# Optimization experiments

Measured on AMD Instinct MI355X. Metric: run time of the kernel, lower is better.

The kernel has to match this reference:

```python
import jax, jax.numpy as jnp
import numpy as np

B, T, D, HS = 4, 2048, 1024, 64

def setup_inputs() -> dict:
    key = jax.random.key(0)
    kx, kk, kq, kv = jax.random.split(key, 4)
    scale = 1.0 / np.sqrt(D)
    return {
        "x": jax.random.normal(kx, (B, T, D), dtype=jnp.float32),
        "Wk": jax.random.normal(kk, (D, HS), dtype=jnp.float32) * scale,
        "Wq": jax.random.normal(kq, (D, HS), dtype=jnp.float32) * scale,
        "Wv": jax.random.normal(kv, (D, HS), dtype=jnp.float32) * scale,
    }

def reference(x, Wk, Wq, Wv):
    # x: [B, T, D]; projections to [B, T, HS]
    k = jnp.einsum("btd,dh->bth", x, Wk)
    q = jnp.einsum("btd,dh->bth", x, Wq)
    v = jnp.einsum("btd,dh->bth", x, Wv)
    # scores [B, T, T]; NOTE: original multiplies by sqrt(head_size) (faithful)
    att = jnp.einsum("bth,bsh->bts", q, k) * jnp.sqrt(jnp.float32(k.shape[-1]))
    Tq = x.shape[1]
    causal = jnp.tril(jnp.ones((Tq, Tq), dtype=bool))
    att = jnp.where(causal[None, :, :], att, -jnp.inf)
    p = jax.nn.softmax(att, axis=-1)
    # dropout = identity (eval mode)
    return jnp.einsum("bts,bsh->bth", p, v)
```

## Files before the change

kernel.cpp:

```cpp
#include <hip/hip_runtime.h>

#define Bn 4
#define Tn 2048
#define Dn 1024
#define HSn 64

typedef __attribute__((ext_vector_type(8))) short bf16x8;
typedef __attribute__((ext_vector_type(4))) float f32x4;
typedef __attribute__((ext_vector_type(4))) short s16x4;
typedef unsigned short u16;
typedef unsigned int u32;

__device__ __forceinline__ u16 f2bf_rne(float x) {
    u32 u = __float_as_uint(x);
    return (u16)((u + 0x7FFFu + ((u >> 16) & 1u)) >> 16);
}
__device__ __forceinline__ u16 f2bf_trunc(float x) {
    return (u16)(__float_as_uint(x) >> 16);
}
__device__ __forceinline__ float bf2f(u16 h) {
    return __uint_as_float(((u32)h) << 16);
}

#define GLL16(g, l)                                                        \
    __builtin_amdgcn_global_load_lds(                                      \
        (const __attribute__((address_space(1))) void*)(g),                \
        (__attribute__((address_space(3))) void*)(l), 16, 0, 0)

__global__ __launch_bounds__(256) void wprep_kernel(
    const float* __restrict__ Wk, const float* __restrict__ Wq,
    const float* __restrict__ Wv, u16* __restrict__ wtp)
{
    __shared__ float ws_[64][65];
    const int kb = blockIdx.x;
    const int w  = blockIdx.y;
    const float* __restrict__ W = (w == 0) ? Wk : (w == 1) ? Wq : Wv;
    const float scale = (w == 1) ? 8.0f : 1.0f;
    const int t = threadIdx.x;

    {
        const int kl = t >> 2, hq = t & 3;
        #pragma unroll
        for (int i = 0; i < 4; ++i) {
            float4 f = *(const float4*)(W + (size_t)(kb * 64 + kl) * 64 + hq * 16 + i * 4);
            ws_[kl][hq * 16 + i * 4 + 0] = f.x; ws_[kl][hq * 16 + i * 4 + 1] = f.y;
            ws_[kl][hq * 16 + i * 4 + 2] = f.z; ws_[kl][hq * 16 + i * 4 + 3] = f.w;
        }
    }
    __syncthreads();

    const int h = t & 63, quarter = t >> 6;
    const int n = w * 64 + h;
    const int ks = kb * 2 + (quarter >> 1);
    const int k_in0 = (quarter & 1) * 16;
    u16 hib[16], lob[16];
    #pragma unroll
    for (int j = 0; j < 16; ++j) {
        float v = ws_[quarter * 16 + j][h] * scale;
        u16 hi = f2bf_trunc(v);
        hib[j] = hi;
        lob[j] = f2bf_trunc(v - bf2f(hi));
    }
    u16* dst = wtp + (size_t)n * 2048 + ks * 64;
    *(uint4*)(dst + k_in0)          = *(const uint4*)&hib[0];
    *(uint4*)(dst + k_in0 + 8)      = *(const uint4*)&hib[8];
    *(uint4*)(dst + 32 + k_in0)     = *(const uint4*)&lob[0];
    *(uint4*)(dst + 32 + k_in0 + 8) = *(const uint4*)&lob[8];
}

#define NKS 32
#define XB(P) (smem + (P) * 4096)
#define BB(P) (smem + 16384 + (P) * 12288)

__global__ __launch_bounds__(256) void proj_gemm(
    const float* __restrict__ x, const u16* __restrict__ wtp,
    u16* __restrict__ qh8, u16* __restrict__ ql8,
    u16* __restrict__ kth, u16* __restrict__ ktl,
    u16* __restrict__ vtt)
{
    __shared__ __align__(16) unsigned char smem[65536];

    const int tid  = threadIdx.x;
    const int wave = tid >> 6, lane = tid & 63;
    const int lo4  = lane & 15, g = lane >> 4;
    const int ch   = blockIdx.x >> 8;
    const int row0 = (blockIdx.x & 255) * 32;
    const int rt   = wave >> 1;
    const int cbase = (wave & 1) * 3;
    const int rl = rt * 16 + lo4;
    const int wcol0 = ch * 96;

    f32x4 acc[3];
    #pragma unroll
    for (int c = 0; c < 3; ++c) acc[c] = (f32x4){0.f, 0.f, 0.f, 0.f};

    const int xr = tid >> 3, xc = tid & 7;
    const int xsw = (xc ^ (xr & 7)) << 2;
    const float* xsrc0 = x + (size_t)(row0 + xr) * Dn + xsw;

    #define STAGE(P, KS)                                                     \
        {                                                                    \
            GLL16(xsrc0 + (KS) * 32, XB(P) + tid * 16);                      \
            _Pragma("unroll")                                                \
            for (int i = 0; i < 3; ++i) {                                    \
                const int c = i * 256 + tid;                                 \
                const int n_ = c >> 3, p_ = c & 7;                           \
                const int l_ = p_ ^ (n_ & 7);                                \
                const u16* src = wtp + (size_t)(wcol0 + n_) * 2048 + (KS) * 64 \
                                 + ((l_ & 3) << 3) + ((l_ >> 2) << 5);       \
                GLL16(src, BB(P) + c * 16);                                  \
            }                                                                \
        }

    #define COMPUTE(P, KS)                                                   \
        {                                                                    \
            bf16x8 ah, al;                                                   \
            {                                                                \
                const unsigned char* xb = XB(P) + rl * 128;                  \
                f32x4 f0 = *(const f32x4*)(xb + (((2 * g + 0) ^ (rl & 7)) << 4)); \
                f32x4 f1 = *(const f32x4*)(xb + (((2 * g + 1) ^ (rl & 7)) << 4)); \
                _Pragma("unroll")                                            \
                for (int jj = 0; jj < 4; ++jj) {                             \
                    u16 h0 = f2bf_trunc(f0[jj]);                             \
                    ah[jj] = (short)h0;                                      \
                    al[jj] = (short)f2bf_trunc(f0[jj] - bf2f(h0));           \
                    u16 h1 = f2bf_trunc(f1[jj]);                             \
                    ah[4 + jj] = (short)h1;                                  \
                    al[4 + jj] = (short)f2bf_trunc(f1[jj] - bf2f(h1));       \
                }                                                            \
            }                                                                \
            _Pragma("unroll")                                                \
            for (int ct = 0; ct < 3; ++ct) {                                 \
                const int n = (cbase + ct) * 16 + lo4;                       \
                const unsigned char* bb = BB(P) + n * 128;                   \
                bf16x8 bh = *(const bf16x8*)(bb + (((g)     ^ (n & 7)) << 4)); \
                bf16x8 bl = *(const bf16x8*)(bb + (((4 + g) ^ (n & 7)) << 4)); \
                acc[ct] = __builtin_amdgcn_mfma_f32_16x16x32_bf16(ah, bh, acc[ct], 0, 0, 0); \
                acc[ct] = __builtin_amdgcn_mfma_f32_16x16x32_bf16(al, bh, acc[ct], 0, 0, 0); \
                acc[ct] = __builtin_amdgcn_mfma_f32_16x16x32_bf16(ah, bl, acc[ct], 0, 0, 0); \
            }                                                                \
        }

    STAGE(0, 0)
    STAGE(1, 1)
    STAGE(2, 2)
    for (int ks = 0; ks < NKS; ++ks) {
        if (ks < NKS - 2) {
            asm volatile("s_waitcnt vmcnt(8)" ::: "memory");
        } else if (ks == NKS - 2) {
            asm volatile("s_waitcnt vmcnt(4)" ::: "memory");
        } else {
            asm volatile("s_waitcnt vmcnt(0)" ::: "memory");
        }
        __builtin_amdgcn_s_barrier();
        asm volatile("" ::: "memory");

        if (ks + 3 < NKS) STAGE((ks + 3) & 3, ks + 3)
        COMPUTE(ks & 3, ks)
    }

    const int grow = row0 + rt * 16 + g * 4;
    const int bb_ = grow >> 11, tl = grow & 2047;
    #pragma unroll
    for (int ct = 0; ct < 3; ++ct) {
        const int n = wcol0 + (cbase + ct) * 16 + lo4;
        if (n < 64) {
            const int kch = n >> 5, gi = (n >> 3) & 3, e = n & 7;
            const size_t base = (size_t)bb_ * 131072
                + (size_t)(((((tl >> 4) * 2 + kch) * 4 + gi) * 16 + (tl & 15)) * 8 + e);
            #pragma unroll
            for (int reg = 0; reg < 4; ++reg) {
                float v = acc[ct][reg];
                u16 hi = f2bf_trunc(v);
                kth[base + reg * 8] = hi;
                ktl[base + reg * 8] = f2bf_trunc(v - bf2f(hi));
            }
        } else if (n < 128) {
            #pragma unroll
            for (int reg = 0; reg < 4; ++reg) {
                float v = acc[ct][reg];
                u16 hi = f2bf_trunc(v);
                qh8[(size_t)(grow + reg) * HSn + (n - 64)] = hi;
                ql8[(size_t)(grow + reg) * HSn + (n - 64)] = f2bf_trunc(v - bf2f(hi));
            }
        } else {
            const int h = n - 128;
            s16x4 pack;
            #pragma unroll
            for (int reg = 0; reg < 4; ++reg)
                pack[reg] = (short)f2bf_rne(acc[ct][reg]);
            const size_t vidx = (size_t)bb_ * 131072
                + (size_t)((tl >> 5) * 2048 + (h >> 4) * 512 + (h & 15) * 32
                           + ((tl >> 3) & 3) * 8 + (tl & 7));
            *(s16x4*)(vtt + vidx) = pack;
        }
    }
}

struct KVset {
    bf16x8 kh0[2], kh1[2], kl0[2], kl1[2], vf[4];
};

__global__ __launch_bounds__(256, 2) void attn_kernel(
    const u16* __restrict__ qh8, const u16* __restrict__ ql8,
    const u16* __restrict__ kth, const u16* __restrict__ ktl,
    const u16* __restrict__ vtt, float* __restrict__ out)
{
    __shared__ __align__(16) unsigned char pbuf[4096];
    __shared__ __align__(16) float om_s[4][16][64];
    __shared__ float ml_s[4][16][2];

    const int tid  = threadIdx.x;
    const int wave = tid >> 6, lane = tid & 63;
    const int lo4  = lane & 15, g = lane >> 4;

    const int sblk = blockIdx.x >> 8, c = blockIdx.x & 255;
    const int tb = sblk ? 127 - (c >> 1) : (c >> 1);
    const int b  = 2 * sblk + (c & 1);
    const int t0 = tb * 16;

    const u16* qhp = qh8 + ((size_t)b * Tn + t0) * HSn;
    const u16* qlp = ql8 + ((size_t)b * Tn + t0) * HSn;
    const u16* kthb = kth + (size_t)b * 131072;
    const u16* ktlb = ktl + (size_t)b * 131072;
    const u16* vttb = vtt + (size_t)b * 131072;
    const int klane = lane * 8;
    const int vlane = lo4 * 32 + g * 8;

    bf16x8 qfh[2], qfl[2];
    #pragma unroll
    for (int ch = 0; ch < 2; ++ch) {
        qfh[ch] = *(const bf16x8*)(qhp + lo4 * HSn + ch * 32 + g * 8);
        qfl[ch] = *(const bf16x8*)(qlp + lo4 * HSn + ch * 32 + g * 8);
    }

    bf16x8 vones;
    #pragma unroll
    for (int i = 0; i < 8; ++i) vones[i] = (short)0x3F80;

    f32x4 O[4];
    #pragma unroll
    for (int n = 0; n < 4; ++n) O[n] = (f32x4){0.f, 0.f, 0.f, 0.f};
    float mrow[4], lrow[4];
    #pragma unroll
    for (int r = 0; r < 4; ++r) { mrow[r] = -1e30f; lrow[r] = 0.f; }

    const int nt = (t0 + 15) / 32 + 1;
    unsigned char* myPB = pbuf + wave * 1024;

    #define LOADSET(S, J)                                                     \
        {                                                                     \
            const u16* kb_ = kthb + (size_t)(2 * (J)) * 1024 + klane;         \
            const u16* lb_ = ktlb + (size_t)(2 * (J)) * 1024 + klane;         \
            S.kh0[0] = *(const bf16x8*)(kb_);                                 \
            S.kh1[0] = *(const bf16x8*)(kb_ + 512);                           \
            S.kh0[1] = *(const bf16x8*)(kb_ + 1024);                          \
            S.kh1[1] = *(const bf16x8*)(kb_ + 1536);                          \
            S.kl0[0] = *(const bf16x8*)(lb_);                                 \
            S.kl1[0] = *(const bf16x8*)(lb_ + 512);                           \
            S.kl0[1] = *(const bf16x8*)(lb_ + 1024);                          \
            S.kl1[1] = *(const bf16x8*)(lb_ + 1536);                          \
            const u16* vb_ = vttb + (size_t)(J) * 2048 + vlane;               \
            S.vf[0] = *(const bf16x8*)(vb_);                                  \
            S.vf[1] = *(const bf16x8*)(vb_ + 512);                            \
            S.vf[2] = *(const bf16x8*)(vb_ + 1024);                           \
            S.vf[3] = *(const bf16x8*)(vb_ + 1536);                           \
        }

    #define COMPUTE_ATT(S, J)                                                 \
        {                                                                     \
            const int s0 = (J) * 32;                                          \
            f32x4 accS[2];                                                    \
            __builtin_amdgcn_s_setprio(1);                                    \
            _Pragma("unroll")                                                 \
            for (int sb = 0; sb < 2; ++sb) {                                  \
                f32x4 a = (f32x4){0.f, 0.f, 0.f, 0.f};                        \
                a = __builtin_amdgcn_mfma_f32_16x16x32_bf16(qfh[0], S.kh0[sb], a, 0, 0, 0); \
                a = __builtin_amdgcn_mfma_f32_16x16x32_bf16(qfh[1], S.kh1[sb], a, 0, 0, 0); \
                a = __builtin_amdgcn_mfma_f32_16x16x32_bf16(qfl[0], S.kh0[sb], a, 0, 0, 0); \
                a = __builtin_amdgcn_mfma_f32_16x16x32_bf16(qfl[1], S.kh1[sb], a, 0, 0, 0); \
                a = __builtin_amdgcn_mfma_f32_16x16x32_bf16(qfh[0], S.kl0[sb], a, 0, 0, 0); \
                a = __builtin_amdgcn_mfma_f32_16x16x32_bf16(qfh[1], S.kl1[sb], a, 0, 0, 0); \
                accS[sb] = a;                                                 \
            }                                                                 \
            __builtin_amdgcn_s_setprio(0);                                    \
            _Pragma("unroll")                                                 \
            for (int reg = 0; reg < 4; ++reg) {                               \
                const int tg  = t0 + g * 4 + reg;                             \
                const int sg0 = s0 + lo4;                                     \
                const int sg1 = s0 + 16 + lo4;                                \
                float v0 = (sg0 <= tg) ? accS[0][reg] : -1e30f;               \
                float v1 = (sg1 <= tg) ? accS[1][reg] : -1e30f;               \
                float mt = fmaxf(v0, v1);                                     \
                mt = fmaxf(mt, __shfl_xor(mt, 1));                            \
                mt = fmaxf(mt, __shfl_xor(mt, 2));                            \
                mt = fmaxf(mt, __shfl_xor(mt, 4));                            \
                mt = fmaxf(mt, __shfl_xor(mt, 8));                            \
                float mn = fmaxf(mrow[reg], mt);                              \
                float p0 = (sg0 <= tg) ? __expf(v0 - mn) : 0.f;               \
                float p1 = (sg1 <= tg) ? __expf(v1 - mn) : 0.f;               \
                float alpha = __expf(mrow[reg] - mn);                         \
                lrow[reg] *= alpha;            \
                mrow[reg] = mn;                                               \
                _Pragma("unroll")                                             \
                for (int n = 0; n < 4; ++n) O[n][reg] *= alpha;               \
                const int irow = g * 4 + reg;                                 \
                *(u16*)(myPB + ((irow * 64 + lo4 * 2) ^ (reg << 4)))      = f2bf_rne(p0); \
                *(u16*)(myPB + ((irow * 64 + 32 + lo4 * 2) ^ (reg << 4))) = f2bf_rne(p1); \
            }                                                                 \
            bf16x8 pf = *(const bf16x8*)(myPB + ((lo4 * 64 + 16 * g) ^ ((lo4 & 3) << 4))); \
            __builtin_amdgcn_s_setprio(1);                                    \
            f32x4 lacc = (f32x4){0.f, 0.f, 0.f, 0.f};                         \
            lacc = __builtin_amdgcn_mfma_f32_16x16x32_bf16(pf, vones, lacc, 0, 0, 0); \
            _Pragma("unroll")                                                 \
            for (int n = 0; n < 4; ++n)                                       \
                O[n] = __builtin_amdgcn_mfma_f32_16x16x32_bf16(pf, S.vf[n], O[n], 0, 0, 0); \
            __builtin_amdgcn_s_setprio(0);                                    \
            _Pragma("unroll")                                                 \
            for (int reg = 0; reg < 4; ++reg) lrow[reg] += lacc[reg];         \
        }

    KVset A, B;
    int j = wave;
    if (j < nt) LOADSET(A, j)
    while (j < nt) {
        if (j + 4 < nt) LOADSET(B, j + 4)
        COMPUTE_ATT(A, j)
        if (j + 4 < nt) {
            if (j + 8 < nt) LOADSET(A, j + 8)
            COMPUTE_ATT(B, j + 4)
        }
        j += 8;
    }

    #pragma unroll
    for (int n = 0; n < 4; ++n)
        #pragma unroll
        for (int reg = 0; reg < 4; ++reg)
            om_s[wave][g * 4 + reg][n * 16 + lo4] = O[n][reg];
    if (lo4 == 0) {
        #pragma unroll
        for (int reg = 0; reg < 4; ++reg) {
            ml_s[wave][g * 4 + reg][0] = mrow[reg];
            ml_s[wave][g * 4 + reg][1] = lrow[reg];
        }
    }
    __syncthreads();

    const int r  = tid >> 4;
    const int h4 = (tid & 15) * 4;
    float mw[4], lw[4], mstar = -1e30f;
    #pragma unroll
    for (int w = 0; w < 4; ++w) {
        mw[w] = ml_s[w][r][0];
        lw[w] = ml_s[w][r][1];
        mstar = fmaxf(mstar, mw[w]);
    }
    float lstar = 0.f, ew[4];
    #pragma unroll
    for (int w = 0; w < 4; ++w) { ew[w] = __expf(mw[w] - mstar); lstar += lw[w] * ew[w]; }
    float4 a4 = {0.f, 0.f, 0.f, 0.f};
    #pragma unroll
    for (int w = 0; w < 4; ++w) {
        float4 t4 = *(const float4*)&om_s[w][r][h4];
        a4.x += t4.x * ew[w]; a4.y += t4.y * ew[w];
        a4.z += t4.z * ew[w]; a4.w += t4.w * ew[w];
    }
    const float inv = 1.f / lstar;
    a4.x *= inv; a4.y *= inv; a4.z *= inv; a4.w *= inv;
    *(float4*)(out + ((size_t)b * Tn + t0 + r) * HSn + h4) = a4;
}

extern "C" void kernel_launch(void* const* d_in, const int* in_sizes, int n_in,
                              void* d_out, int out_size, void* d_ws, size_t ws_size,
                              hipStream_t stream) {
    const float* x  = (const float*)d_in[0];
    const float* Wk = (const float*)d_in[1];
    const float* Wq = (const float*)d_in[2];
    const float* Wv = (const float*)d_in[3];
    float* out = (float*)d_out;

    const size_t per = (size_t)Bn * Tn * HSn;
    u16* qh8 = (u16*)d_ws;
    u16* ql8 = qh8 + per;
    u16* kth = ql8 + per;
    u16* ktl = kth + per;
    u16* vtt = ktl + per;
    u16* wtp = vtt + per;

    hipLaunchKernelGGL(wprep_kernel, dim3(16, 3), dim3(256), 0, stream,
                       Wk, Wq, Wv, wtp);
    hipLaunchKernelGGL(proj_gemm, dim3(512), dim3(256), 0, stream,
                       x, wtp, qh8, ql8, kth, ktl, vtt);
    hipLaunchKernelGGL(attn_kernel, dim3(512), dim3(256), 0, stream,
                       qh8, ql8, kth, ktl, vtt, out);
}
```

Baseline: 46.42 us.

## Load projection GEMM operands straight to registers with MFMA-fragment weight layout

The projection GEMM drops its LDS staging (global_load_lds, barriers, swizzled reads) and has each wave load x and weight fragments directly into registers, double-buffered across k-steps. Weights are pre-packed by wprep into a layout matching the MFMA B-fragment so each lane does contiguous 16-byte loads. Each block now covers 16 rows across all 192 output columns, with 4 waves taking 3 column tiles each, and MFMA issue priority is raised. The aim is to remove LDS traffic and barrier overhead. In exchange, x rows are re-read by every wave with no shared reuse and latency hiding relies on register prefetch only.

Measured after the change: 57.20 us. 1.23x slower.

```diff
diff --git a/kernel.cpp b/kernel.cpp
--- a/kernel.cpp
+++ b/kernel.cpp
@@ -22,14 +22,9 @@
     return __uint_as_float(((u32)h) << 16);
 }
 
-#define GLL16(g, l)                                                        \
-    __builtin_amdgcn_global_load_lds(                                      \
-        (const __attribute__((address_space(1))) void*)(g),                \
-        (__attribute__((address_space(3))) void*)(l), 16, 0, 0)
-
 __global__ __launch_bounds__(256) void wprep_kernel(
     const float* __restrict__ Wk, const float* __restrict__ Wq,
-    const float* __restrict__ Wv, u16* __restrict__ wtp)
+    const float* __restrict__ Wv, u16* __restrict__ wtp2)
 {
     __shared__ float ws_[64][65];
     const int kb = blockIdx.x;
@@ -50,9 +45,8 @@
     __syncthreads();
 
     const int h = t & 63, quarter = t >> 6;
-    const int n = w * 64 + h;
-    const int ks = kb * 2 + (quarter >> 1);
-    const int k_in0 = (quarter & 1) * 16;
+    const int nt = w * 4 + (h >> 4);
+    const int ksub = quarter >> 1;
     u16 hib[16], lob[16];
     #pragma unroll
     for (int j = 0; j < 16; ++j) {
@@ -61,109 +55,90 @@
         hib[j] = hi;
         lob[j] = f2bf_trunc(v - bf2f(hi));
     }
-    u16* dst = wtp + (size_t)n * 2048 + ks * 64;
-    *(uint4*)(dst + k_in0)          = *(const uint4*)&hib[0];
-    *(uint4*)(dst + k_in0 + 8)      = *(const uint4*)&hib[8];
-    *(uint4*)(dst + 32 + k_in0)     = *(const uint4*)&lob[0];
-    *(uint4*)(dst + 32 + k_in0 + 8) = *(const uint4*)&lob[8];
+    const int lane0 = ((quarter * 2 + 0) & 3) * 16 + (h & 15);
+    const int lane1 = ((quarter * 2 + 1) & 3) * 16 + (h & 15);
+    u16* base = wtp2 + (size_t)kb * 24576 + (size_t)(ksub * 12 + nt) * 1024;
+    *(uint4*)(base + lane0 * 8)       = *(const uint4*)&hib[0];
+    *(uint4*)(base + lane1 * 8)       = *(const uint4*)&hib[8];
+    *(uint4*)(base + 512 + lane0 * 8) = *(const uint4*)&lob[0];
+    *(uint4*)(base + 512 + lane1 * 8) = *(const uint4*)&lob[8];
 }
 
 #define NKS 32
-#define XB(P) (smem + (P) * 4096)
-#define BB(P) (smem + 16384 + (P) * 12288)
+
+struct Pset {
+    f32x4 xa, xb;
+    bf16x8 bh[3], bl[3];
+};
 
 __global__ __launch_bounds__(256) void proj_gemm(
-    const float* __restrict__ x, const u16* __restrict__ wtp,
+    const float* __restrict__ x, const u16* __restrict__ wtp2,
     u16* __restrict__ qh8, u16* __restrict__ ql8,
     u16* __restrict__ kth, u16* __restrict__ ktl,
     u16* __restrict__ vtt)
 {
-    __shared__ __align__(16) unsigned char smem[65536];
-
     const int tid  = threadIdx.x;
     const int wave = tid >> 6, lane = tid & 63;
     const int lo4  = lane & 15, g = lane >> 4;
-    const int ch   = blockIdx.x >> 8;
-    const int row0 = (blockIdx.x & 255) * 32;
-    const int rt   = wave >> 1;
-    const int cbase = (wave & 1) * 3;
-    const int rl = rt * 16 + lo4;
-    const int wcol0 = ch * 96;
+    const int row0 = blockIdx.x * 16;
+    const int nt0  = wave * 3;
 
     f32x4 acc[3];
     #pragma unroll
     for (int c = 0; c < 3; ++c) acc[c] = (f32x4){0.f, 0.f, 0.f, 0.f};
 
-    const int xr = tid >> 3, xc = tid & 7;
-    const int xsw = (xc ^ (xr & 7)) << 2;
-    const float* xsrc0 = x + (size_t)(row0 + xr) * Dn + xsw;
-
-    #define STAGE(P, KS)                                                     \
-        {                                                                    \
-            GLL16(xsrc0 + (KS) * 32, XB(P) + tid * 16);                      \
-            _Pragma("unroll")                                                \
-            for (int i = 0; i < 3; ++i) {                                    \
-                const int c = i * 256 + tid;                                 \
-                const int n_ = c >> 3, p_ = c & 7;                           \
-                const int l_ = p_ ^ (n_ & 7);                                \
-                const u16* src = wtp + (size_t)(wcol0 + n_) * 2048 + (KS) * 64 \
-                                 + ((l_ & 3) << 3) + ((l_ >> 2) << 5);       \
-                GLL16(src, BB(P) + c * 16);                                  \
-            }                                                                \
-        }
-
-    #define COMPUTE(P, KS)                                                   \
+    const float* ap0 = x + (size_t)(row0 + lo4) * Dn + g * 8;
+    const u16*   bp0 = wtp2 + (size_t)nt0 * 1024 + lane * 8;
+
+    #define LOADP(S, KS)                                                      \
+        {                                                                     \
+            const float* ap = ap0 + (KS) * 32;                                \
+            S.xa = *(const f32x4*)(ap);                                       \
+            S.xb = *(const f32x4*)(ap + 4);                                   \
+            const u16* bp = bp0 + (size_t)(KS) * 12288;                       \
+            _Pragma("unroll")                                                 \
+            for (int ct = 0; ct < 3; ++ct) {                                  \
+                S.bh[ct] = *(const bf16x8*)(bp + ct * 1024);                  \
+                S.bl[ct] = *(const bf16x8*)(bp + ct * 1024 + 512);            \
+            }                                                                 \
+        }
+
+    #define COMPUTEP(S)                                                      \
         {                                                                    \
             bf16x8 ah, al;                                                   \
-            {                                                                \
-                const unsigned char* xb = XB(P) + rl * 128;                  \
-                f32x4 f0 = *(const f32x4*)(xb + (((2 * g + 0) ^ (rl & 7)) << 4)); \
-                f32x4 f1 = *(const f32x4*)(xb + (((2 * g + 1) ^ (rl & 7)) << 4)); \
-                _Pragma("unroll")                                            \
-                for (int jj = 0; jj < 4; ++jj) {                             \
-                    u16 h0 = f2bf_trunc(f0[jj]);                             \
-                    ah[jj] = (short)h0;                                      \
-                    al[jj] = (short)f2bf_trunc(f0[jj] - bf2f(h0));           \
-                    u16 h1 = f2bf_trunc(f1[jj]);                             \
-                    ah[4 + jj] = (short)h1;                                  \
-                    al[4 + jj] = (short)f2bf_trunc(f1[jj] - bf2f(h1));       \
-                }                                                            \
+            _Pragma("unroll")                                                \
+            for (int jj = 0; jj < 4; ++jj) {                                 \
+                u16 h0 = f2bf_trunc(S.xa[jj]);                               \
+                ah[jj] = (short)h0;                                          \
+                al[jj] = (short)f2bf_trunc(S.xa[jj] - bf2f(h0));             \
+                u16 h1 = f2bf_trunc(S.xb[jj]);                               \
+                ah[4 + jj] = (short)h1;                                      \
+                al[4 + jj] = (short)f2bf_trunc(S.xb[jj] - bf2f(h1));         \
             }                                                                \
+            __builtin_amdgcn_s_setprio(1);                                   \
             _Pragma("unroll")                                                \
             for (int ct = 0; ct < 3; ++ct) {                                 \
-                const int n = (cbase + ct) * 16 + lo4;                       \
-                const unsigned char* bb = BB(P) + n * 128;                   \
-                bf16x8 bh = *(const bf16x8*)(bb + (((g)     ^ (n & 7)) << 4)); \
-                bf16x8 bl = *(const bf16x8*)(bb + (((4 + g) ^ (n & 7)) << 4)); \
-                acc[ct] = __builtin_amdgcn_mfma_f32_16x16x32_bf16(ah, bh, acc[ct], 0, 0, 0); \
-                acc[ct] = __builtin_amdgcn_mfma_f32_16x16x32_bf16(al, bh, acc[ct], 0, 0, 0); \
-                acc[ct] = __builtin_amdgcn_mfma_f32_16x16x32_bf16(ah, bl, acc[ct], 0, 0, 0); \
+                acc[ct] = __builtin_amdgcn_mfma_f32_16x16x32_bf16(ah, S.bh[ct], acc[ct], 0, 0, 0); \
+                acc[ct] = __builtin_amdgcn_mfma_f32_16x16x32_bf16(al, S.bh[ct], acc[ct], 0, 0, 0); \
+                acc[ct] = __builtin_amdgcn_mfma_f32_16x16x32_bf16(ah, S.bl[ct], acc[ct], 0, 0, 0); \
             }                                                                \
-        }
-
-    STAGE(0, 0)
-    STAGE(1, 1)
-    STAGE(2, 2)
-    for (int ks = 0; ks < NKS; ++ks) {
-        if (ks < NKS - 2) {
-            asm volatile("s_waitcnt vmcnt(8)" ::: "memory");
-        } else if (ks == NKS - 2) {
-            asm volatile("s_waitcnt vmcnt(4)" ::: "memory");
-        } else {
-            asm volatile("s_waitcnt vmcnt(0)" ::: "memory");
-        }
-        __builtin_amdgcn_s_barrier();
-        asm volatile("" ::: "memory");
-
-        if (ks + 3 < NKS) STAGE((ks + 3) & 3, ks + 3)
-        COMPUTE(ks & 3, ks)
-    }
-
-    const int grow = row0 + rt * 16 + g * 4;
+            __builtin_amdgcn_s_setprio(0);                                   \
+        }
+
+    Pset A, B;
+    LOADP(A, 0)
+    for (int ks = 0; ks < NKS; ks += 2) {
+        LOADP(B, ks + 1)
+        COMPUTEP(A)
+        if (ks + 2 < NKS) LOADP(A, ks + 2)
+        COMPUTEP(B)
+    }
+
+    const int grow = row0 + g * 4;
     const int bb_ = grow >> 11, tl = grow & 2047;
     #pragma unroll
     for (int ct = 0; ct < 3; ++ct) {
-        const int n = wcol0 + (cbase + ct) * 16 + lo4;
+        const int n = (nt0 + ct) * 16 + lo4;
         if (n < 64) {
             const int kch = n >> 5, gi = (n >> 3) & 3, e = n & 7;
             const size_t base = (size_t)bb_ * 131072
@@ -386,12 +361,12 @@
     u16* kth = ql8 + per;
     u16* ktl = kth + per;
     u16* vtt = ktl + per;
-    u16* wtp = vtt + per;
+    u16* wtp2 = vtt + per;
 
     hipLaunchKernelGGL(wprep_kernel, dim3(16, 3), dim3(256), 0, stream,
-                       Wk, Wq, Wv, wtp);
+                       Wk, Wq, Wv, wtp2);
     hipLaunchKernelGGL(proj_gemm, dim3(512), dim3(256), 0, stream,
-                       x, wtp, qh8, ql8, kth, ktl, vtt);
+                       x, wtp2, qh8, ql8, kth, ktl, vtt);
     hipLaunchKernelGGL(attn_kernel, dim3(512), dim3(256), 0, stream,
                        qh8, ql8, kth, ktl, vtt, out);
 }
```
